# Kernel optimization log

Measured on AMD Instinct MI355X. Metric: run time of the kernel, lower is better.

Reference implementation:

```python
import jax, jax.numpy as jnp
import numpy as np
import math

D_MODEL = 1024
NUM_HEADS = 16
HEAD_DIM = D_MODEL // NUM_HEADS


def setup_inputs() -> dict:
    key = jax.random.key(0)
    ks = jax.random.split(key, 9)
    B, S = 2, 2048
    scale = 1.0 / math.sqrt(D_MODEL)
    x = jax.random.normal(ks[0], (B, S, D_MODEL), dtype=jnp.float32)
    # torch nn.Linear params: weight [out, in], bias [out]
    Wq = jax.random.normal(ks[1], (D_MODEL, D_MODEL), dtype=jnp.float32) * scale
    bq = jax.random.normal(ks[2], (D_MODEL,), dtype=jnp.float32) * scale
    Wk = jax.random.normal(ks[3], (D_MODEL, D_MODEL), dtype=jnp.float32) * scale
    bk = jax.random.normal(ks[4], (D_MODEL,), dtype=jnp.float32) * scale
    Wv = jax.random.normal(ks[5], (D_MODEL, D_MODEL), dtype=jnp.float32) * scale
    bv = jax.random.normal(ks[6], (D_MODEL,), dtype=jnp.float32) * scale
    Wo = jax.random.normal(ks[7], (D_MODEL, D_MODEL), dtype=jnp.float32) * scale
    bo = jax.random.normal(ks[8], (D_MODEL,), dtype=jnp.float32) * scale
    return {"x": x, "Wq": Wq, "bq": bq, "Wk": Wk, "bk": bk,
            "Wv": Wv, "bv": bv, "Wo": Wo, "bo": bo}


def reference(x, Wq, bq, Wk, bk, Wv, bv, Wo, bo):
    B, S, _ = x.shape
    H, Dh = NUM_HEADS, HEAD_DIM

    def proj(W, b):
        # torch Linear: x @ W.T + b -> [B,S,D] -> [B,H,S,Dh]
        y = jnp.einsum('bsd,ed->bse', x, W) + b
        return y.reshape(B, S, H, Dh).transpose(0, 2, 1, 3)

    Q = proj(Wq, bq)
    K = proj(Wk, bk)
    V = proj(Wv, bv)

    # scores [B,H,S,S], causal mask with -inf, then scale by 1/sqrt(head_dim)
    scores = jnp.einsum('bhqd,bhkd->bhqk', Q, K)
    causal = jnp.tril(jnp.ones((S, S), dtype=bool))
    scores = jnp.where(causal, scores, -jnp.inf)
    A = jax.nn.softmax(scores / math.sqrt(Dh), axis=-1)

    O = jnp.einsum('bhqk,bhkd->bhqd', A, V)  # [B,H,S,Dh]
    O = O.transpose(0, 2, 1, 3).reshape(B, S, H * Dh)
    return jnp.einsum('bsd,ed->bse', O, Wo) + bo
```

## Files before the change

### kernel.cpp

```cpp
#include <hip/hip_runtime.h>


typedef _Float16 f16x8 __attribute__((ext_vector_type(8)));
typedef _Float16 f16x4 __attribute__((ext_vector_type(4)));
typedef _Float16 f16x2 __attribute__((ext_vector_type(2)));
typedef float f32x4 __attribute__((ext_vector_type(4)));

#define S_  2048
#define DM  1024
#define NH  16
#define DH  64

__device__ __forceinline__ void gload_lds16(const void* g, void* s) {
  __builtin_amdgcn_global_load_lds(
      (const __attribute__((address_space(1))) void*)g,
      (__attribute__((address_space(3))) void*)s, 16, 0, 0);
}

__device__ __forceinline__ f16x2 pkrtz(float a, float b) {
  return __builtin_bit_cast(f16x2, __builtin_amdgcn_cvt_pkrtz(a, b));
}


__global__ void cvt_all_kernel(const float* __restrict__ x,
                               const float* __restrict__ w0,
                               const float* __restrict__ w1,
                               const float* __restrict__ w2,
                               const float* __restrict__ w3,
                               _Float16* __restrict__ xb,
                               _Float16* __restrict__ wb) {
  const int bid = blockIdx.x;
  const float* src;
  _Float16* dst;
  int idx;
  if (bid < 4096) {
    src = x; dst = xb; idx = bid * 256 + threadIdx.x;
  } else {
    const int j = bid - 4096;
    const int y = j >> 10;
    src = (y == 0) ? w0 : (y == 1) ? w1 : (y == 2) ? w2 : w3;
    dst = wb + (size_t)y * (DM * DM);
    idx = (j & 1023) * 256 + threadIdx.x;
  }
  const float4 v = ((const float4*)src)[idx];
  f16x4 h;
  h[0] = (_Float16)v.x; h[1] = (_Float16)v.y;
  h[2] = (_Float16)v.z; h[3] = (_Float16)v.w;
  ((f16x4*)dst)[idx] = h;
}


__global__ __launch_bounds__(256, 2) void gemm_qkv_kernel(
    const _Float16* __restrict__ xb, const _Float16* __restrict__ wb,
    const float* __restrict__ bq, const float* __restrict__ bk,
    const float* __restrict__ bv, _Float16* __restrict__ qkv)
{
  __shared__ _Float16 As[2][128 * 32];
  __shared__ _Float16 Ws[2][128 * 32];
  const int z = blockIdx.z;
  const _Float16* W = wb + (size_t)z * (DM * DM);
  const float* bias = (z == 0) ? bq : ((z == 1) ? bk : bv);
  _Float16* out = qkv + (size_t)z * 4194304;

  const f32x4 z4 = {0.f, 0.f, 0.f, 0.f};
  f32x4 acc[4][4];
#pragma unroll
  for (int mi = 0; mi < 4; ++mi)
#pragma unroll
    for (int ni = 0; ni < 4; ++ni) acc[mi][ni] = z4;

  const int m0 = blockIdx.y * 128, n0 = blockIdx.x * 128;
  const int t = threadIdx.x;
  const int w = t >> 6, l = t & 63;
  const int quad = l >> 4, ln = l & 15;
  const int wm = (w >> 1) << 6, wn = (w & 1) << 6;
  const int srow = l >> 2, scol = (l & 3) << 3;

  for (int k0 = 0; k0 < DM; k0 += 64) {
#pragma unroll
    for (int h = 0; h < 2; ++h)
#pragma unroll
      for (int i = 0; i < 2; ++i) {
        const int ra = w * 32 + i * 16;
        gload_lds16(&xb[(size_t)(m0 + ra + srow) * DM + k0 + h * 32 + scol],
                    &As[h][ra * 32]);
        gload_lds16(&W[(size_t)(n0 + ra + srow) * DM + k0 + h * 32 + scol],
                    &Ws[h][ra * 32]);
      }
    __syncthreads();

#pragma unroll
    for (int h = 0; h < 2; ++h) {
      f16x8 af[4], bf[4];
#pragma unroll
      for (int mi = 0; mi < 4; ++mi)
        af[mi] = *(const f16x8*)&As[h][(wm + mi * 16 + ln) * 32 + quad * 8];
#pragma unroll
      for (int ni = 0; ni < 4; ++ni)
        bf[ni] = *(const f16x8*)&Ws[h][(wn + ni * 16 + ln) * 32 + quad * 8];
#pragma unroll
      for (int mi = 0; mi < 4; ++mi)
#pragma unroll
        for (int ni = 0; ni < 4; ++ni)
          acc[mi][ni] = __builtin_amdgcn_mfma_f32_16x16x32_f16(
              af[mi], bf[ni], acc[mi][ni], 0, 0, 0);
    }
    __syncthreads();
  }

  const float scale = (z == 0) ? 0.18033688f : 1.0f;

#pragma unroll
  for (int ni = 0; ni < 4; ++ni) {
    const int c = n0 + wn + ni * 16 + ln;
    const float bias_c = bias[c];
    const int h = c >> 6, d = c & 63;
#pragma unroll
    for (int mi = 0; mi < 4; ++mi) {
      const int mb = m0 + wm + mi * 16 + quad * 4;
#pragma unroll
      for (int r = 0; r < 4; ++r) {
        const int mg = mb + r;
        const int b = mg >> 11, s = mg & 2047;
        const int bh = b * NH + h;
        const float v = (acc[mi][ni][r] + bias_c) * scale;
        size_t idx;
        if (z == 2)
          idx = (size_t)bh * 131072 + (s >> 5) * 2048 + (d >> 4) * 512 +
                ((s >> 3) & 3) * 128 + (d & 15) * 8 + (s & 7);
        else
          idx = (size_t)bh * 131072 + (s >> 4) * 1024 + (d >> 5) * 512 +
                ((d >> 3) & 3) * 128 + (s & 15) * 8 + (d & 7);
        out[idx] = (_Float16)v;
      }
    }
  }
}


__global__ __launch_bounds__(256, 2) void gemm_out_kernel(
    const _Float16* __restrict__ ob, const _Float16* __restrict__ wo,
    const float* __restrict__ bo, float* __restrict__ out)
{
  __shared__ _Float16 As[2][128 * 32];
  __shared__ _Float16 Ws[2][64 * 32];
  const f32x4 z4 = {0.f, 0.f, 0.f, 0.f};
  f32x4 acc[2][4];
#pragma unroll
  for (int mi = 0; mi < 2; ++mi)
#pragma unroll
    for (int ni = 0; ni < 4; ++ni) acc[mi][ni] = z4;

  const int m0 = blockIdx.y * 128, n0 = blockIdx.x * 64;
  const int t = threadIdx.x;
  const int w = t >> 6, l = t & 63;
  const int quad = l >> 4, ln = l & 15;
  const int srow = l >> 2, scol = (l & 3) << 3;

  for (int k0 = 0; k0 < DM; k0 += 64) {
#pragma unroll
    for (int h = 0; h < 2; ++h) {
#pragma unroll
      for (int i = 0; i < 2; ++i) {
        const int ra = w * 32 + i * 16;
        gload_lds16(&ob[(size_t)(m0 + ra + srow) * DM + k0 + h * 32 + scol],
                    &As[h][ra * 32]);
      }
      gload_lds16(&wo[(size_t)(n0 + w * 16 + srow) * DM + k0 + h * 32 + scol],
                  &Ws[h][w * 16 * 32]);
    }
    __syncthreads();

#pragma unroll
    for (int h = 0; h < 2; ++h) {
      f16x8 af[2], bf[4];
#pragma unroll
      for (int mi = 0; mi < 2; ++mi)
        af[mi] = *(const f16x8*)&As[h][(w * 32 + mi * 16 + ln) * 32 + quad * 8];
#pragma unroll
      for (int ni = 0; ni < 4; ++ni)
        bf[ni] = *(const f16x8*)&Ws[h][(ni * 16 + ln) * 32 + quad * 8];
#pragma unroll
      for (int mi = 0; mi < 2; ++mi)
#pragma unroll
        for (int ni = 0; ni < 4; ++ni)
          acc[mi][ni] = __builtin_amdgcn_mfma_f32_16x16x32_f16(
              af[mi], bf[ni], acc[mi][ni], 0, 0, 0);
    }
    __syncthreads();
  }

#pragma unroll
  for (int ni = 0; ni < 4; ++ni) {
    const int c = n0 + ni * 16 + ln;
    const float bias_c = bo[c];
#pragma unroll
    for (int mi = 0; mi < 2; ++mi) {
      const int mb = m0 + w * 32 + mi * 16 + quad * 4;
#pragma unroll
      for (int r = 0; r < 4; ++r)
        out[(size_t)(mb + r) * DM + c] = acc[mi][ni][r] + bias_c;
    }
  }
}


template <bool DIAG>
__device__ __forceinline__ void compute_tile(
    const _Float16* __restrict__ kb_, const _Float16* __restrict__ vb_,
    int t, const f16x8 (&qf)[2][2], f32x4 (&oacc)[4][2],
    float (&l_i)[2], _Float16* Ps, int quad, int ln, int l)
{
  f16x8 kf[4], vf[4];
#pragma unroll
  for (int i = 0; i < 4; ++i)
    kf[i] = *(const f16x8*)(kb_ + (size_t)(t * 4 + i) * 512 + l * 8);
#pragma unroll
  for (int i = 0; i < 4; ++i)
    vf[i] = *(const f16x8*)(vb_ + (size_t)(t * 4 + i) * 512 + l * 8);

  const f32x4 z4 = {0.f, 0.f, 0.f, 0.f};
  f32x4 sacc[2][2];
#pragma unroll
  for (int mi = 0; mi < 2; ++mi)
#pragma unroll
    for (int qc = 0; qc < 2; ++qc) sacc[mi][qc] = z4;

#pragma unroll
  for (int ks = 0; ks < 2; ++ks)
#pragma unroll
    for (int mi = 0; mi < 2; ++mi)
#pragma unroll
      for (int qc = 0; qc < 2; ++qc)
        sacc[mi][qc] = __builtin_amdgcn_mfma_f32_16x16x32_f16(
            kf[mi * 2 + ks], qf[qc][ks], sacc[mi][qc], 0, 0, 0);

  const int sw = (ln & 3) << 1;
#pragma unroll
  for (int qc = 0; qc < 2; ++qc) {
    float rs = 0.f;
#pragma unroll
    for (int mi = 0; mi < 2; ++mi) {
      float p[4];
#pragma unroll
      for (int r = 0; r < 4; ++r) {
        p[r] = __builtin_amdgcn_exp2f(sacc[mi][qc][r]);
        if (DIAG && (mi * 16 + quad * 4 + r > qc * 16 + ln)) p[r] = 0.f;
        rs += p[r];
      }
      const f16x2 lo = pkrtz(p[0], p[1]);
      const f16x2 hi = pkrtz(p[2], p[3]);
      const f16x4 pk = __builtin_shufflevector(lo, hi, 0, 1, 2, 3);
      const int g = (mi * 4 + quad) ^ sw;
      *(f16x4*)&Ps[(qc * 16 + ln) * 40 + g * 4] = pk;
    }
    l_i[qc] += rs;
  }

  f16x8 pb[2];
#pragma unroll
  for (int qc = 0; qc < 2; ++qc) {
    const int g2 = (quad * 2) ^ sw;
    pb[qc] = *(const f16x8*)&Ps[(qc * 16 + ln) * 40 + g2 * 4];
  }

#pragma unroll
  for (int di = 0; di < 4; ++di)
#pragma unroll
    for (int qc = 0; qc < 2; ++qc)
      oacc[di][qc] = __builtin_amdgcn_mfma_f32_16x16x32_f16(
          vf[di], pb[qc], oacc[di][qc], 0, 0, 0);
}

__global__ __launch_bounds__(256, 4) void attn_kernel(
    const _Float16* __restrict__ QF, const _Float16* __restrict__ KF,
    const _Float16* __restrict__ VF, _Float16* __restrict__ Ob)
{
  __shared__ _Float16 Ps[4 * 32 * 40];
  __shared__ float mrg[3 * 64 * 34];

  const int i = blockIdx.x;
  const int bh = ((i & 7) << 2) | ((i >> 3) & 3);
  const int p = i >> 5;

  const int tid = threadIdx.x;
  const int w = tid >> 6, l = tid & 63;
  const int quad = l >> 4, ln = l & 15;

  const _Float16* qb_ = QF + (size_t)bh * 131072;
  const _Float16* kb_ = KF + (size_t)bh * 131072;
  const _Float16* vb_ = VF + (size_t)bh * 131072;
  _Float16* psw = Ps + w * (32 * 40);
  const int bidx = bh >> 4, h = bh & 15;

  const f32x4 z4 = {0.f, 0.f, 0.f, 0.f};

#pragma unroll
  for (int mem = 0; mem < 2; ++mem) {
    const int qw = (mem == 0) ? (63 - p) : p;
    const int q0 = qw << 5;

    f16x8 qf[2][2];
#pragma unroll
    for (int qc = 0; qc < 2; ++qc)
#pragma unroll
      for (int ks = 0; ks < 2; ++ks)
        qf[qc][ks] = *(const f16x8*)
            (qb_ + (size_t)((2 * qw + qc) * 2 + ks) * 512 + l * 8);

    f32x4 oacc[4][2];
#pragma unroll
    for (int di = 0; di < 4; ++di)
#pragma unroll
      for (int qc = 0; qc < 2; ++qc) oacc[di][qc] = z4;
    float l_i[2] = {0.f, 0.f};

    int t = w;
    for (; t < qw; t += 4)
      compute_tile<false>(kb_, vb_, t, qf, oacc, l_i, psw, quad, ln, l);
    if (t == qw)
      compute_tile<true>(kb_, vb_, t, qf, oacc, l_i, psw, quad, ln, l);

#pragma unroll
    for (int qc = 0; qc < 2; ++qc) {
      float s = l_i[qc];
      s += __shfl_xor(s, 16);
      s += __shfl_xor(s, 32);
      l_i[qc] = s;
    }

    if (w != 0) {
      float* m_ = &mrg[((w - 1) * 64 + l) * 34];
#pragma unroll
      for (int di = 0; di < 4; ++di)
#pragma unroll
        for (int qc = 0; qc < 2; ++qc)
          *(f32x4*)(m_ + di * 8 + qc * 4) = oacc[di][qc];
      m_[32] = l_i[0];
      m_[33] = l_i[1];
    }
    __syncthreads();
    if (w == 0) {
#pragma unroll
      for (int ww = 0; ww < 3; ++ww) {
        const float* m_ = &mrg[(ww * 64 + l) * 34];
#pragma unroll
        for (int di = 0; di < 4; ++di)
#pragma unroll
          for (int qc = 0; qc < 2; ++qc)
            oacc[di][qc] += *(const f32x4*)(m_ + di * 8 + qc * 4);
        l_i[0] += m_[32];
        l_i[1] += m_[33];
      }
#pragma unroll
      for (int qc = 0; qc < 2; ++qc) {
        const float inv = 1.0f / l_i[qc];
        const int q = q0 + qc * 16 + ln;
        _Float16* orow = Ob + (size_t)(bidx * S_ + q) * DM + h * DH + quad * 4;
#pragma unroll
        for (int di = 0; di < 4; ++di) {
          f16x4 o4;
#pragma unroll
          for (int r = 0; r < 4; ++r)
            o4[r] = (_Float16)(oacc[di][qc][r] * inv);
          *(f16x4*)(orow + di * 16) = o4;
        }
      }
    }
    __syncthreads();
  }
}


extern "C" void kernel_launch(void* const* d_in, const int* in_sizes, int n_in,
                              void* d_out, int out_size, void* d_ws, size_t ws_size,
                              hipStream_t stream) {
  (void)in_sizes; (void)n_in; (void)out_size; (void)ws_size;
  const float* x  = (const float*)d_in[0];
  const float* Wq = (const float*)d_in[1];
  const float* bq = (const float*)d_in[2];
  const float* Wk = (const float*)d_in[3];
  const float* bk = (const float*)d_in[4];
  const float* Wv = (const float*)d_in[5];
  const float* bv = (const float*)d_in[6];
  const float* Wo = (const float*)d_in[7];
  const float* bo = (const float*)d_in[8];

  char* ws = (char*)d_ws;
  _Float16* xb  = (_Float16*)(ws);
  _Float16* wb  = (_Float16*)(ws + (8u << 20));
  _Float16* qkv = (_Float16*)(ws + (16u << 20));
  _Float16* ob  = (_Float16*)(ws + (40u << 20));

  cvt_all_kernel<<<dim3(8192), dim3(256), 0, stream>>>(x, Wq, Wk, Wv, Wo, xb, wb);
  gemm_qkv_kernel<<<dim3(8, 32, 3), dim3(256), 0, stream>>>(xb, wb, bq, bk, bv, qkv);
  attn_kernel<<<dim3(1024), dim3(256), 0, stream>>>(
      qkv, qkv + 4194304, qkv + 2 * 4194304, ob);
  gemm_out_kernel<<<dim3(16, 32), dim3(256), 0, stream>>>(
      ob, wb + (size_t)3 * DM * DM, bo, (float*)d_out);
}
```

Before: 178.9 us.

## Split attention work per wave by query half instead of key tiles

Each wave now owns one 16-row query half of one of the block's two query tiles and walks every key tile itself. This removes the cross-wave LDS merge, the merge buffer and both block barriers. The role is rotated with the block index to spread load, and the next K tile is prefetched into registers while the current one is processed. In exchange each wave reads K/V tiles that other waves in the block also read, so redundant global traffic rises. Per-wave work also becomes uneven, since early and late query tiles differ in length.

Result: slower. 187.0 us (+4.5%).

```diff
diff --git a/kernel.cpp b/kernel.cpp
--- a/kernel.cpp
+++ b/kernel.cpp
@@ -206,78 +206,61 @@
 
 
 template <bool DIAG>
-__device__ __forceinline__ void compute_tile(
-    const _Float16* __restrict__ kb_, const _Float16* __restrict__ vb_,
-    int t, const f16x8 (&qf)[2][2], f32x4 (&oacc)[4][2],
-    float (&l_i)[2], _Float16* Ps, int quad, int ln, int l)
+__device__ __forceinline__ void tile16(
+    const _Float16* __restrict__ vb_, int t,
+    const f16x8 (&kc)[4], const f16x8 (&qf)[2],
+    f32x4 (&oacc)[4], float& l_i,
+    _Float16* Ps, int quad, int ln, int l, int h)
 {
-  f16x8 kf[4], vf[4];
-#pragma unroll
-  for (int i = 0; i < 4; ++i)
-    kf[i] = *(const f16x8*)(kb_ + (size_t)(t * 4 + i) * 512 + l * 8);
+  f16x8 vf[4];
 #pragma unroll
   for (int i = 0; i < 4; ++i)
     vf[i] = *(const f16x8*)(vb_ + (size_t)(t * 4 + i) * 512 + l * 8);
 
   const f32x4 z4 = {0.f, 0.f, 0.f, 0.f};
-  f32x4 sacc[2][2];
-#pragma unroll
-  for (int mi = 0; mi < 2; ++mi)
-#pragma unroll
-    for (int qc = 0; qc < 2; ++qc) sacc[mi][qc] = z4;
+  f32x4 sacc[2];
+  sacc[0] = z4; sacc[1] = z4;
 
 #pragma unroll
   for (int ks = 0; ks < 2; ++ks)
 #pragma unroll
     for (int mi = 0; mi < 2; ++mi)
-#pragma unroll
-      for (int qc = 0; qc < 2; ++qc)
-        sacc[mi][qc] = __builtin_amdgcn_mfma_f32_16x16x32_f16(
-            kf[mi * 2 + ks], qf[qc][ks], sacc[mi][qc], 0, 0, 0);
+      sacc[mi] = __builtin_amdgcn_mfma_f32_16x16x32_f16(
+          kc[mi * 2 + ks], qf[ks], sacc[mi], 0, 0, 0);
 
   const int sw = (ln & 3) << 1;
-#pragma unroll
-  for (int qc = 0; qc < 2; ++qc) {
-    float rs = 0.f;
-#pragma unroll
-    for (int mi = 0; mi < 2; ++mi) {
-      float p[4];
-#pragma unroll
-      for (int r = 0; r < 4; ++r) {
-        p[r] = __builtin_amdgcn_exp2f(sacc[mi][qc][r]);
-        if (DIAG && (mi * 16 + quad * 4 + r > qc * 16 + ln)) p[r] = 0.f;
-        rs += p[r];
-      }
-      const f16x2 lo = pkrtz(p[0], p[1]);
-      const f16x2 hi = pkrtz(p[2], p[3]);
-      const f16x4 pk = __builtin_shufflevector(lo, hi, 0, 1, 2, 3);
-      const int g = (mi * 4 + quad) ^ sw;
-      *(f16x4*)&Ps[(qc * 16 + ln) * 40 + g * 4] = pk;
-    }
-    l_i[qc] += rs;
-  }
-
-  f16x8 pb[2];
-#pragma unroll
-  for (int qc = 0; qc < 2; ++qc) {
-    const int g2 = (quad * 2) ^ sw;
-    pb[qc] = *(const f16x8*)&Ps[(qc * 16 + ln) * 40 + g2 * 4];
-  }
+  float rs = 0.f;
+#pragma unroll
+  for (int mi = 0; mi < 2; ++mi) {
+    float p[4];
+#pragma unroll
+    for (int r = 0; r < 4; ++r) {
+      p[r] = __builtin_amdgcn_exp2f(sacc[mi][r]);
+      if (DIAG && (mi * 16 + quad * 4 + r > h * 16 + ln)) p[r] = 0.f;
+      rs += p[r];
+    }
+    const f16x2 lo = pkrtz(p[0], p[1]);
+    const f16x2 hi = pkrtz(p[2], p[3]);
+    const f16x4 pk = __builtin_shufflevector(lo, hi, 0, 1, 2, 3);
+    const int g = (mi * 4 + quad) ^ sw;
+    *(f16x4*)&Ps[ln * 40 + g * 4] = pk;
+  }
+  l_i += rs;
+
+  const int g2 = (quad * 2) ^ sw;
+  const f16x8 pb = *(const f16x8*)&Ps[ln * 40 + g2 * 4];
 
 #pragma unroll
   for (int di = 0; di < 4; ++di)
-#pragma unroll
-    for (int qc = 0; qc < 2; ++qc)
-      oacc[di][qc] = __builtin_amdgcn_mfma_f32_16x16x32_f16(
-          vf[di], pb[qc], oacc[di][qc], 0, 0, 0);
+    oacc[di] = __builtin_amdgcn_mfma_f32_16x16x32_f16(
+        vf[di], pb, oacc[di], 0, 0, 0);
 }
 
 __global__ __launch_bounds__(256, 4) void attn_kernel(
     const _Float16* __restrict__ QF, const _Float16* __restrict__ KF,
     const _Float16* __restrict__ VF, _Float16* __restrict__ Ob)
 {
-  __shared__ _Float16 Ps[4 * 32 * 40];
-  __shared__ float mrg[3 * 64 * 34];
+  __shared__ _Float16 Ps[4 * 16 * 40];
 
   const int i = blockIdx.x;
   const int bh = ((i & 7) << 2) | ((i >> 3) & 3);
@@ -287,87 +270,58 @@
   const int w = tid >> 6, l = tid & 63;
   const int quad = l >> 4, ln = l & 15;
 
+  const int role = (w + (i >> 8)) & 3;
+  const int qw = (role < 2) ? (63 - p) : p;
+  const int h = role & 1;
+
   const _Float16* qb_ = QF + (size_t)bh * 131072;
   const _Float16* kb_ = KF + (size_t)bh * 131072;
   const _Float16* vb_ = VF + (size_t)bh * 131072;
-  _Float16* psw = Ps + w * (32 * 40);
-  const int bidx = bh >> 4, h = bh & 15;
+  _Float16* psw = Ps + w * (16 * 40);
+  const int bidx = bh >> 4, hh = bh & 15;
+
+  f16x8 qf[2];
+#pragma unroll
+  for (int ks = 0; ks < 2; ++ks)
+    qf[ks] = *(const f16x8*)
+        (qb_ + (size_t)((qw * 2 + h) * 2 + ks) * 512 + l * 8);
 
   const f32x4 z4 = {0.f, 0.f, 0.f, 0.f};
-
-#pragma unroll
-  for (int mem = 0; mem < 2; ++mem) {
-    const int qw = (mem == 0) ? (63 - p) : p;
-    const int q0 = qw << 5;
-
-    f16x8 qf[2][2];
-#pragma unroll
-    for (int qc = 0; qc < 2; ++qc)
-#pragma unroll
-      for (int ks = 0; ks < 2; ++ks)
-        qf[qc][ks] = *(const f16x8*)
-            (qb_ + (size_t)((2 * qw + qc) * 2 + ks) * 512 + l * 8);
-
-    f32x4 oacc[4][2];
-#pragma unroll
-    for (int di = 0; di < 4; ++di)
-#pragma unroll
-      for (int qc = 0; qc < 2; ++qc) oacc[di][qc] = z4;
-    float l_i[2] = {0.f, 0.f};
-
-    int t = w;
-    for (; t < qw; t += 4)
-      compute_tile<false>(kb_, vb_, t, qf, oacc, l_i, psw, quad, ln, l);
-    if (t == qw)
-      compute_tile<true>(kb_, vb_, t, qf, oacc, l_i, psw, quad, ln, l);
-
-#pragma unroll
-    for (int qc = 0; qc < 2; ++qc) {
-      float s = l_i[qc];
-      s += __shfl_xor(s, 16);
-      s += __shfl_xor(s, 32);
-      l_i[qc] = s;
-    }
-
-    if (w != 0) {
-      float* m_ = &mrg[((w - 1) * 64 + l) * 34];
-#pragma unroll
-      for (int di = 0; di < 4; ++di)
-#pragma unroll
-        for (int qc = 0; qc < 2; ++qc)
-          *(f32x4*)(m_ + di * 8 + qc * 4) = oacc[di][qc];
-      m_[32] = l_i[0];
-      m_[33] = l_i[1];
-    }
-    __syncthreads();
-    if (w == 0) {
-#pragma unroll
-      for (int ww = 0; ww < 3; ++ww) {
-        const float* m_ = &mrg[(ww * 64 + l) * 34];
-#pragma unroll
-        for (int di = 0; di < 4; ++di)
-#pragma unroll
-          for (int qc = 0; qc < 2; ++qc)
-            oacc[di][qc] += *(const f32x4*)(m_ + di * 8 + qc * 4);
-        l_i[0] += m_[32];
-        l_i[1] += m_[33];
-      }
-#pragma unroll
-      for (int qc = 0; qc < 2; ++qc) {
-        const float inv = 1.0f / l_i[qc];
-        const int q = q0 + qc * 16 + ln;
-        _Float16* orow = Ob + (size_t)(bidx * S_ + q) * DM + h * DH + quad * 4;
-#pragma unroll
-        for (int di = 0; di < 4; ++di) {
-          f16x4 o4;
-#pragma unroll
-          for (int r = 0; r < 4; ++r)
-            o4[r] = (_Float16)(oacc[di][qc][r] * inv);
-          *(f16x4*)(orow + di * 16) = o4;
-        }
-      }
-    }
-    __syncthreads();
+  f32x4 oacc[4];
+#pragma unroll
+  for (int di = 0; di < 4; ++di) oacc[di] = z4;
+  float l_i = 0.f;
+
+  f16x8 kc[4];
+#pragma unroll
+  for (int ii = 0; ii < 4; ++ii)
+    kc[ii] = *(const f16x8*)(kb_ + (size_t)ii * 512 + l * 8);
+
+  for (int t = 0; t < qw; ++t) {
+    f16x8 kn[4];
+#pragma unroll
+    for (int ii = 0; ii < 4; ++ii)
+      kn[ii] = *(const f16x8*)
+          (kb_ + (size_t)((t + 1) * 4 + ii) * 512 + l * 8);
+    tile16<false>(vb_, t, kc, qf, oacc, l_i, psw, quad, ln, l, h);
+#pragma unroll
+    for (int ii = 0; ii < 4; ++ii) kc[ii] = kn[ii];
+  }
+  tile16<true>(vb_, qw, kc, qf, oacc, l_i, psw, quad, ln, l, h);
+
+  l_i += __shfl_xor(l_i, 16);
+  l_i += __shfl_xor(l_i, 32);
+  const float inv = 1.0f / l_i;
+
+  const int q = qw * 32 + h * 16 + ln;
+  _Float16* orow = Ob + (size_t)(bidx * S_ + q) * DM + hh * DH + quad * 4;
+#pragma unroll
+  for (int di = 0; di < 4; ++di) {
+    f16x4 o4;
+#pragma unroll
+    for (int r = 0; r < 4; ++r)
+      o4[r] = (_Float16)(oacc[di][r] * inv);
+    *(f16x4*)(orow + di * 16) = o4;
   }
 }
 
```
